# Performance work log

Hardware: AMD Instinct MI355X
Metric: run time of the kernel (lower is better)

## Reference

```python
import jax, jax.numpy as jnp
import numpy as np

N = 50_000
HS = 256
H = 256  # GAT heads (hard-coded in module)
E12 = 250_000
E3 = 500_000


def _gat(x, edge, W, a_src, a_dst, b):
    # PyG GATConv(1, 1, heads=256, concat=False, add_self_loops=False)
    n = x.shape[0]
    xl = x @ W                                   # [N,1]@[1,H] -> [N,H] (out_channels=1 per head)
    src, dst = edge[0], edge[1]
    alpha = jax.nn.leaky_relu((xl * a_src)[src] + (xl * a_dst)[dst], 0.2)  # [E,H]
    amax = jax.ops.segment_max(alpha, dst, num_segments=n)
    ex = jnp.exp(alpha - amax[dst])
    den = jax.ops.segment_sum(ex, dst, num_segments=n)
    w = ex / (den[dst] + 1e-16)                  # per-dst softmax (PyG softmax eps)
    out = jax.ops.segment_sum(xl[src] * w, dst, num_segments=n)            # [N,H]
    return jnp.mean(out, axis=1, keepdims=True) + b                        # concat=False -> head mean


def _sage(x, edge, Wl, Wr):
    # PyG SAGEConv, mean aggregation, root_weight=True, bias=False
    n = x.shape[0]
    src, dst = edge[0], edge[1]
    agg = jax.ops.segment_sum(x[src], dst, num_segments=n)
    cnt = jax.ops.segment_sum(jnp.ones((src.shape[0], 1), x.dtype), dst, num_segments=n)
    return (agg / jnp.maximum(cnt, 1.0)) @ Wl + x @ Wr


def _forward(floats, r1, r2, r3, neg):
    (x, fc1_w, fc1_b, fc2_w, fc2_b, fc3_w, fc3_b,
     g1_w, g1_as, g1_ad, g1_b, g2_w, g2_as, g2_ad, g2_b, g3_w, g3_as, g3_ad, g3_b,
     sg1_wl, sg1_wr, sg2_wl, sg2_wr, sg3_wl, sg3_wr, c21_wl, c21_wr,
     fc4_w, fc4_b, fc4n_w, fc4n_b, fc5_w, fc5_b, fc6_w, fc6_b, fc7_w, fc7_b) = floats
    relu = jax.nn.relu
    x_price = x[:, :1]
    h = relu(x[:, 1:] @ fc1_w + fc1_b)
    h = relu(h @ fc2_w + fc2_b)
    x3 = relu(h @ fc3_w + fc3_b)
    p1 = relu(_gat(x_price, r1, g1_w, g1_as, g1_ad, g1_b))
    p2 = relu(_gat(x_price, r2, g2_w, g2_as, g2_ad, g2_b))
    p3 = relu(_gat(x_price, r3, g3_w, g3_as, g3_ad, g3_b))
    x1 = jnp.concatenate([x3, p1, p2, p3], axis=1)           # [N, hs+3]
    s = jnp.concatenate([
        relu(_sage(x1, r3, sg1_wl, sg1_wr)),
        relu(_sage(x1, r3, sg2_wl, sg2_wr)),
        relu(_sage(x1, r3, sg3_wl, sg3_wr)),
    ], axis=1)                                               # [N, 3*(hs>>1)]
    y = relu(s @ fc4_w + fc4_b)
    y = relu(y @ fc5_w + fc5_b)
    y = y @ fc6_w + fc6_b
    xn = relu(_sage(x1, neg, c21_wl, c21_wr))
    xn = relu(xn @ fc4n_w + fc4n_b)
    xn = xn @ fc7_w + fc7_b
    return (y, xn)


def setup_inputs() -> dict:
    key = jax.random.key(0)
    ks = iter(jax.random.split(key, 64))
    def nrm(shape, s=0.05):
        return jax.random.normal(next(ks), shape, jnp.float32) * s
    def rint(shape, hi):
        return jax.random.randint(next(ks), shape, 0, hi, jnp.int32)
    inp = {
        'x': jax.random.normal(next(ks), (N, 19), jnp.float32),
        'fc1_w': nrm((18, HS)), 'fc1_b': nrm((HS,)),
        'fc2_w': nrm((HS, HS)), 'fc2_b': nrm((HS,)),
        'fc3_w': nrm((HS, HS)), 'fc3_b': nrm((HS,)),
        'g1_w': nrm((1, H)), 'g1_as': nrm((H,)), 'g1_ad': nrm((H,)), 'g1_b': nrm((1,)),
        'g2_w': nrm((1, H)), 'g2_as': nrm((H,)), 'g2_ad': nrm((H,)), 'g2_b': nrm((1,)),
        'g3_w': nrm((1, H)), 'g3_as': nrm((H,)), 'g3_ad': nrm((H,)), 'g3_b': nrm((1,)),
        'sg1_wl': nrm((HS + 3, HS // 2)), 'sg1_wr': nrm((HS + 3, HS // 2)),
        'sg2_wl': nrm((HS + 3, HS // 2)), 'sg2_wr': nrm((HS + 3, HS // 2)),
        'sg3_wl': nrm((HS + 3, HS // 2)), 'sg3_wr': nrm((HS + 3, HS // 2)),
        'c21_wl': nrm((HS + 3, HS)), 'c21_wr': nrm((HS + 3, HS)),
        'fc4_w': nrm((3 * (HS // 2), HS)), 'fc4_b': nrm((HS,)),
        'fc4n_w': nrm((HS, HS)), 'fc4n_b': nrm((HS,)),
        'fc5_w': nrm((HS, HS)), 'fc5_b': nrm((HS,)),
        'fc6_w': nrm((HS, 1)), 'fc6_b': nrm((1,)),
        'fc7_w': nrm((HS, 1)), 'fc7_b': nrm((1,)),
        'r1_edge_index': rint((2, E12), N),
        'r2_edge_index': rint((2, E12), N),
        'r3_edge_index': rint((2, E3), N),
        'neg_edge_index': rint((2, E3), N),
    }
    return inp


def reference(x, fc1_w, fc1_b, fc2_w, fc2_b, fc3_w, fc3_b,
              g1_w, g1_as, g1_ad, g1_b, g2_w, g2_as, g2_ad, g2_b,
              g3_w, g3_as, g3_ad, g3_b,
              sg1_wl, sg1_wr, sg2_wl, sg2_wr, sg3_wl, sg3_wr, c21_wl, c21_wr,
              fc4_w, fc4_b, fc4n_w, fc4n_b, fc5_w, fc5_b, fc6_w, fc6_b, fc7_w, fc7_b,
              r1_edge_index, r2_edge_index, r3_edge_index, neg_edge_index):
    floats = (x, fc1_w, fc1_b, fc2_w, fc2_b, fc3_w, fc3_b,
              g1_w, g1_as, g1_ad, g1_b, g2_w, g2_as, g2_ad, g2_b, g3_w, g3_as, g3_ad, g3_b,
              sg1_wl, sg1_wr, sg2_wl, sg2_wr, sg3_wl, sg3_wr, c21_wl, c21_wr,
              fc4_w, fc4_b, fc4n_w, fc4n_b, fc5_w, fc5_b, fc6_w, fc6_b, fc7_w, fc7_b)
    return _forward(floats, r1_edge_index, r2_edge_index, r3_edge_index, neg_edge_index)
```

## Files before the change

kernel.cpp:

```cpp
#include <hip/hip_runtime.h>
#include <hip/hip_bf16.h>

typedef __hip_bfloat16 bf16;
typedef __attribute__((ext_vector_type(8))) short bfrag;
typedef __attribute__((ext_vector_type(4))) float f32x4;

static constexpr int NN  = 50000;
static constexpr int EA  = 250000;
static constexpr int EB  = 500000;
static constexpr int LDX = 288;

__device__ __forceinline__ float b2f(unsigned int u) { return __uint_as_float((u & 0xffffu) << 16); }
__device__ __forceinline__ unsigned short f2b(float f) {
    bf16 h = __float2bfloat16(f);
    return *reinterpret_cast<unsigned short*>(&h);
}
__device__ __forceinline__ void gload16(const void* g, void* l) {
    __builtin_amdgcn_global_load_lds((const __attribute__((address_space(1))) void*)g,
                                     (__attribute__((address_space(3))) void*)l, 16, 0, 0);
}

__global__ void k_zero(unsigned int* __restrict__ p, int n) {
    int i = blockIdx.x * 256 + threadIdx.x;
    if (i < n) p[i] = 0u;
}

__global__ void k_count(const int* __restrict__ dst, int E, int* __restrict__ deg) {
    int e = blockIdx.x * blockDim.x + threadIdx.x;
    if (e < E) atomicAdd(&deg[dst[e]], 1);
}

__global__ __launch_bounds__(1024) void k_scan4(const int* __restrict__ deg4,
                                                int* __restrict__ rp4,
                                                int* __restrict__ cur4, int n) {
    const int* deg = deg4 + (size_t)blockIdx.x * n;
    int* rp  = rp4  + (size_t)blockIdx.x * (n + 1);
    int* cur = cur4 + (size_t)blockIdx.x * n;
    __shared__ int wsum[16];
    __shared__ int srun;
    int tid = threadIdx.x;
    int lane = tid & 63, wid = tid >> 6;
    if (tid == 0) srun = 0;
    __syncthreads();
    for (int base = 0; base < n; base += 1024) {
        int i = base + tid;
        int v = (i < n) ? deg[i] : 0;
        int incl = v;
        #pragma unroll
        for (int d = 1; d < 64; d <<= 1) {
            int y = __shfl_up(incl, d, 64);
            if (lane >= d) incl += y;
        }
        if (lane == 63) wsum[wid] = incl;
        __syncthreads();
        if (wid == 0 && lane < 16) {
            int w = wsum[lane];
            #pragma unroll
            for (int d = 1; d < 16; d <<= 1) {
                int y = __shfl_up(w, d, 64);
                if (lane >= d) w += y;
            }
            wsum[lane] = w;
        }
        __syncthreads();
        int run  = srun;
        int woff = (wid > 0) ? wsum[wid - 1] : 0;
        int ex   = run + woff + incl - v;
        if (i < n) { rp[i] = ex; cur[i] = ex; }
        int total = wsum[15];
        __syncthreads();
        if (tid == 0) srun = run + total;
        __syncthreads();
    }
    if (tid == 0) rp[n] = srun;
}

__global__ void k_scatter(const int* __restrict__ src, const int* __restrict__ dst, int E,
                          int* __restrict__ cur, int* __restrict__ col) {
    int e = blockIdx.x * blockDim.x + threadIdx.x;
    if (e < E) {
        int p = atomicAdd(&cur[dst[e]], 1);
        col[p] = src[e];
    }
}

__global__ __launch_bounds__(256) void k_fc1(const float* __restrict__ x,
                                             const float* __restrict__ W,
                                             const float* __restrict__ bias,
                                             bf16* __restrict__ out) {
    __shared__ float sx[8][20];
    int tid = threadIdx.x;
    int n0 = blockIdx.x * 8;
    for (int i = tid; i < 8 * 19; i += 256) {
        int m = i / 19, k = i % 19;
        sx[m][k] = x[(size_t)(n0 + m) * 19 + k];
    }
    __syncthreads();
    float wr[18];
    #pragma unroll
    for (int k = 0; k < 18; ++k) wr[k] = W[k * 256 + tid];
    float bv = bias[tid];
    #pragma unroll
    for (int m = 0; m < 8; ++m) {
        float acc = bv;
        #pragma unroll
        for (int k = 0; k < 18; ++k) acc = fmaf(sx[m][k + 1], wr[k], acc);
        out[(size_t)(n0 + m) * 256 + tid] = __float2bfloat16(fmaxf(acc, 0.f));
    }
}

__global__ __launch_bounds__(256) void k_mgemm(
    const bf16* __restrict__ A1, int lda1, int K1,
    const bf16* __restrict__ A2, int lda2, int K2,
    const bf16* __restrict__ WT,
    const float* __restrict__ bias,
    bf16* __restrict__ C, int ldc, int M,
    const float* __restrict__ vdot, float* __restrict__ dotout)
{
    __shared__ char lds[16384] __attribute__((aligned(16)));
    const int tid  = threadIdx.x;
    const int lane = tid & 63;
    const int wid  = tid >> 6;
    const int wm   = wid >> 1, wn = wid & 1;
    const int row0 = blockIdx.y * 128;
    const int col0 = blockIdx.x * 128;
    const int Ktot = K1 + K2;
    const int lmod = lane & 15;
    const int ldiv = lane >> 4;

    f32x4 acc[4][4] = {};

    const bool doA  = (wid < 2);
    const int cbase = (wid & 1) * 4;

    for (int kb = 0; kb < Ktot; kb += 32) {
        __syncthreads();
        if (doA) {
            const bf16* Ap; int lda, kk;
            if (kb < K1) { Ap = A1; lda = lda1; kk = kb; }
            else         { Ap = A2; lda = lda2; kk = kb - K1; }
            int kcol = kk + ldiv * 8;
            #pragma unroll
            for (int c = 0; c < 4; ++c) {
                int chunk = cbase + c;
                int row = row0 + chunk * 16 + lmod;
                row = row < M ? row : M - 1;
                gload16(Ap + (size_t)row * lda + kcol, lds + chunk * 1024);
            }
        } else {
            int kcol = kb + ldiv * 8;
            #pragma unroll
            for (int c = 0; c < 4; ++c) {
                int chunk = cbase + c;
                int col = col0 + chunk * 16 + lmod;
                gload16(WT + (size_t)col * Ktot + kcol, lds + 8192 + chunk * 1024);
            }
        }
        __syncthreads();
        bfrag a[4], b[4];
        #pragma unroll
        for (int i = 0; i < 4; ++i)
            a[i] = *(const bfrag*)(lds + (wm * 4 + i) * 1024 + lane * 16);
        #pragma unroll
        for (int i = 0; i < 4; ++i)
            b[i] = *(const bfrag*)(lds + 8192 + (wn * 4 + i) * 1024 + lane * 16);
        #pragma unroll
        for (int mi = 0; mi < 4; ++mi)
            #pragma unroll
            for (int ni = 0; ni < 4; ++ni)
                acc[mi][ni] = __builtin_amdgcn_mfma_f32_16x16x32_bf16(a[mi], b[ni], acc[mi][ni], 0, 0, 0);
    }

    float bv[4], vv[4];
    #pragma unroll
    for (int ni = 0; ni < 4; ++ni) {
        int colv = col0 + wn * 64 + ni * 16 + lmod;
        bv[ni] = bias ? bias[colv] : 0.f;
        vv[ni] = vdot ? vdot[colv] : 0.f;
    }

    if (vdot) {
        #pragma unroll
        for (int mi = 0; mi < 4; ++mi) {
            #pragma unroll
            for (int r = 0; r < 4; ++r) {
                int row = row0 + wm * 64 + mi * 16 + ldiv * 4 + r;
                float part = 0.f;
                #pragma unroll
                for (int ni = 0; ni < 4; ++ni)
                    part = fmaf(fmaxf(acc[mi][ni][r] + bv[ni], 0.f), vv[ni], part);
                #pragma unroll
                for (int d = 1; d < 16; d <<= 1) part += __shfl_xor(part, d, 64);
                if (lmod == 0 && row < M) atomicAdd(&dotout[row], part);
            }
        }
        return;
    }

    #pragma unroll
    for (int mi = 0; mi < 4; ++mi) {
        int rowb = row0 + wm * 64 + mi * 16 + ldiv * 4;
        #pragma unroll
        for (int ni = 0; ni < 4; ++ni) {
            int col = col0 + wn * 64 + ni * 16 + lmod;
            #pragma unroll
            for (int r = 0; r < 4; ++r) {
                int row = rowb + r;
                if (row < M)
                    C[(size_t)row * ldc + col] = __float2bfloat16(fmaxf(acc[mi][ni][r] + bv[ni], 0.f));
            }
        }
    }
}

__global__ __launch_bounds__(256) void k_gat(
    const float* __restrict__ x,
    const int* __restrict__ rp, const int* __restrict__ col,
    const float* __restrict__ gw, const float* __restrict__ gas,
    const float* __restrict__ gad, const float* __restrict__ gb,
    bf16* __restrict__ x1, int outcol)
{
    int lane = threadIdx.x & 63;
    int node = blockIdx.x * 4 + (threadIdx.x >> 6);
    if (node >= NN) return;
    int beg = rp[node], end = rp[node + 1];
    float bias = gb[0];
    float res;
    if (end == beg) {
        res = fmaxf(bias, 0.f);
    } else {
        float maxa = -3.4e38f, mina = 3.4e38f;
        for (int e = beg + lane; e < end; e += 64) {
            float a = x[(size_t)col[e] * 19];
            maxa = fmaxf(maxa, a);
            mina = fminf(mina, a);
        }
        #pragma unroll
        for (int d = 32; d >= 1; d >>= 1) {
            maxa = fmaxf(maxa, __shfl_xor(maxa, d, 64));
            mina = fminf(mina, __shfl_xor(mina, d, 64));
        }
        float b = x[(size_t)node * 19];
        float w[4], u[4], cc[4];
        #pragma unroll
        for (int j = 0; j < 4; ++j) {
            float wv = gw[lane * 4 + j];
            w[j]  = wv;
            u[j]  = wv * gas[lane * 4 + j];
            cc[j] = b * wv * gad[lane * 4 + j];
        }
        float m[4], s[4], t[4];
        #pragma unroll
        for (int j = 0; j < 4; ++j) {
            float sel = (u[j] >= 0.f) ? maxa : mina;
            float mm = fmaf(sel, u[j], cc[j]);
            m[j] = (mm >= 0.f) ? mm : 0.2f * mm;
            s[j] = 0.f; t[j] = 0.f;
        }
        for (int e = beg; e < end; ++e) {
            float a = x[(size_t)col[e] * 19];
            #pragma unroll
            for (int j = 0; j < 4; ++j) {
                float al = fmaf(a, u[j], cc[j]);
                al = (al >= 0.f) ? al : 0.2f * al;
                float p = __expf(al - m[j]);
                s[j] += p;
                t[j] += p * a;
            }
        }
        float part = 0.f;
        #pragma unroll
        for (int j = 0; j < 4; ++j) part += w[j] * t[j] / (s[j] + 1e-16f);
        #pragma unroll
        for (int d = 32; d >= 1; d >>= 1) part += __shfl_xor(part, d, 64);
        res = fmaxf(part * (1.f / 256.f) + bias, 0.f);
    }
    if (lane == 0) x1[(size_t)node * LDX + outcol] = __float2bfloat16(res);
}

__global__ __launch_bounds__(256) void k_sage_agg(
    const bf16* __restrict__ x1, const int* __restrict__ rp, const int* __restrict__ col,
    bf16* __restrict__ agg)
{
    int lane = threadIdx.x & 63;
    int node = blockIdx.x * 4 + (threadIdx.x >> 6);
    if (node >= NN) return;
    int beg = rp[node], end = rp[node + 1];
    float inv = 1.f / fmaxf((float)(end - beg), 1.f);
    if (lane >= 36) return;
    float s0=0,s1=0,s2=0,s3=0,s4=0,s5=0,s6=0,s7=0;
    for (int e = beg; e < end; ++e) {
        const uint4 v = *(const uint4*)(x1 + (size_t)col[e] * LDX + lane * 8);
        s0 += b2f(v.x); s1 += b2f(v.x >> 16);
        s2 += b2f(v.y); s3 += b2f(v.y >> 16);
        s4 += b2f(v.z); s5 += b2f(v.z >> 16);
        s6 += b2f(v.w); s7 += b2f(v.w >> 16);
    }
    uint4 o;
    o.x = (unsigned)f2b(s0 * inv) | ((unsigned)f2b(s1 * inv) << 16);
    o.y = (unsigned)f2b(s2 * inv) | ((unsigned)f2b(s3 * inv) << 16);
    o.z = (unsigned)f2b(s4 * inv) | ((unsigned)f2b(s5 * inv) << 16);
    o.w = (unsigned)f2b(s6 * inv) | ((unsigned)f2b(s7 * inv) << 16);
    *(uint4*)(agg + (size_t)node * LDX + lane * 8) = o;
}

__global__ void k_final(const float* __restrict__ dots,
                        const float* __restrict__ b6, const float* __restrict__ b7,
                        float* __restrict__ out) {
    int i = blockIdx.x * 256 + threadIdx.x;
    if (i >= 2 * NN) return;
    float b = (i < NN) ? b6[0] : b7[0];
    out[i] = dots[i] + b;
}

__global__ void k_wt(const float* __restrict__ W, bf16* __restrict__ WT, int K, int N) {
    int idx = blockIdx.x * 256 + threadIdx.x;
    if (idx >= K * N) return;
    int n = idx / K, k = idx % K;
    WT[idx] = __float2bfloat16(W[k * N + n]);
}

__global__ void k_wtsage(const float* __restrict__ wl0, const float* __restrict__ wl1,
                         const float* __restrict__ wl2, const float* __restrict__ wr0,
                         const float* __restrict__ wr1, const float* __restrict__ wr2,
                         bf16* __restrict__ WT) {
    int idx = blockIdx.x * 256 + threadIdx.x;
    if (idx >= 384 * 576) return;
    int n = idx / 576, k = idx % 576;
    int half = k / 288, kk = k % 288;
    float v = 0.f;
    if (kk < 259) {
        const float* s = half ? (n < 128 ? wr0 : n < 256 ? wr1 : wr2)
                              : (n < 128 ? wl0 : n < 256 ? wl1 : wl2);
        v = s[kk * 128 + (n & 127)];
    }
    WT[idx] = __float2bfloat16(v);
}

__global__ void k_wtc21(const float* __restrict__ wl, const float* __restrict__ wr,
                        bf16* __restrict__ WT) {
    int idx = blockIdx.x * 256 + threadIdx.x;
    if (idx >= 256 * 576) return;
    int n = idx / 576, k = idx % 576;
    int half = k / 288, kk = k % 288;
    float v = 0.f;
    if (kk < 259) v = (half ? wr : wl)[kk * 256 + n];
    WT[idx] = __float2bfloat16(v);
}

__global__ void k_padx1(bf16* __restrict__ x1) {
    int idx = blockIdx.x * 256 + threadIdx.x;
    if (idx >= NN * 32) return;
    int node = idx >> 5, c = idx & 31;
    x1[(size_t)node * LDX + 256 + c] = __float2bfloat16(0.f);
}

extern "C" void kernel_launch(void* const* d_in, const int* in_sizes, int n_in,
                              void* d_out, int out_size, void* d_ws, size_t ws_size,
                              hipStream_t stream)
{
    (void)in_sizes; (void)n_in; (void)out_size; (void)ws_size;
    const float* x      = (const float*)d_in[0];
    const float* fc1_w  = (const float*)d_in[1];
    const float* fc1_b  = (const float*)d_in[2];
    const float* fc2_w  = (const float*)d_in[3];
    const float* fc2_b  = (const float*)d_in[4];
    const float* fc3_w  = (const float*)d_in[5];
    const float* fc3_b  = (const float*)d_in[6];
    const float* g_w[3]  = {(const float*)d_in[7],  (const float*)d_in[11], (const float*)d_in[15]};
    const float* g_as[3] = {(const float*)d_in[8],  (const float*)d_in[12], (const float*)d_in[16]};
    const float* g_ad[3] = {(const float*)d_in[9],  (const float*)d_in[13], (const float*)d_in[17]};
    const float* g_b[3]  = {(const float*)d_in[10], (const float*)d_in[14], (const float*)d_in[18]};
    const float* sg_wl[3] = {(const float*)d_in[19], (const float*)d_in[21], (const float*)d_in[23]};
    const float* sg_wr[3] = {(const float*)d_in[20], (const float*)d_in[22], (const float*)d_in[24]};
    const float* c21_wl = (const float*)d_in[25];
    const float* c21_wr = (const float*)d_in[26];
    const float* fc4_w  = (const float*)d_in[27];
    const float* fc4_b  = (const float*)d_in[28];
    const float* fc4n_w = (const float*)d_in[29];
    const float* fc4n_b = (const float*)d_in[30];
    const float* fc5_w  = (const float*)d_in[31];
    const float* fc5_b  = (const float*)d_in[32];
    const float* fc6_w  = (const float*)d_in[33];
    const float* fc6_b  = (const float*)d_in[34];
    const float* fc7_w  = (const float*)d_in[35];
    const float* fc7_b  = (const float*)d_in[36];
    const int* eidx[4] = {(const int*)d_in[37], (const int*)d_in[38], (const int*)d_in[39], (const int*)d_in[40]};
    const int  ecnt[4] = {EA, EA, EB, EB};

    bf16* bws = (bf16*)d_ws;
    size_t off = 0;
    bf16* x1    = bws + off; off += (size_t)NN * LDX;
    bf16* bufA  = bws + off; off += (size_t)NN * LDX;
    bf16* bufB  = bws + off; off += (size_t)NN * 384;
    bf16* fc2T  = bws + off; off += 256 * 256;
    bf16* fc3T  = bws + off; off += 256 * 256;
    bf16* fc4T  = bws + off; off += 256 * 384;
    bf16* fc4nT = bws + off; off += 256 * 256;
    bf16* fc5T  = bws + off; off += 256 * 256;
    bf16* sageT = bws + off; off += 384 * 576;
    bf16* c21T  = bws + off; off += 256 * 576;
    float* dots = (float*)(bws + off);
    int* deg4 = (int*)(dots + 2 * NN);
    int* rp4  = deg4 + 4 * NN;
    int* cur4 = rp4 + 4 * (NN + 1);
    int* colx = cur4 + 4 * NN;
    int* colg[4] = {colx, colx + EA, colx + 2 * EA, colx + 2 * EA + EB};

    float* outy = (float*)d_out;

    k_zero<<<(4 * NN + 255) / 256, 256, 0, stream>>>((unsigned int*)deg4, 4 * NN);
    k_zero<<<(2 * NN + 255) / 256, 256, 0, stream>>>((unsigned int*)dots, 2 * NN);

    for (int g = 0; g < 4; ++g)
        k_count<<<(ecnt[g] + 255) / 256, 256, 0, stream>>>(eidx[g] + ecnt[g], ecnt[g], deg4 + g * NN);
    k_scan4<<<4, 1024, 0, stream>>>(deg4, rp4, cur4, NN);
    for (int g = 0; g < 4; ++g)
        k_scatter<<<(ecnt[g] + 255) / 256, 256, 0, stream>>>(eidx[g], eidx[g] + ecnt[g], ecnt[g],
                                                             cur4 + g * NN, colg[g]);

    k_wt<<<(256 * 256 + 255) / 256, 256, 0, stream>>>(fc2_w, fc2T, 256, 256);
    k_wt<<<(256 * 256 + 255) / 256, 256, 0, stream>>>(fc3_w, fc3T, 256, 256);
    k_wt<<<(384 * 256 + 255) / 256, 256, 0, stream>>>(fc4_w, fc4T, 384, 256);
    k_wt<<<(256 * 256 + 255) / 256, 256, 0, stream>>>(fc4n_w, fc4nT, 256, 256);
    k_wt<<<(256 * 256 + 255) / 256, 256, 0, stream>>>(fc5_w, fc5T, 256, 256);
    k_wtsage<<<(384 * 576 + 255) / 256, 256, 0, stream>>>(sg_wl[0], sg_wl[1], sg_wl[2],
                                                          sg_wr[0], sg_wr[1], sg_wr[2], sageT);
    k_wtc21<<<(256 * 576 + 255) / 256, 256, 0, stream>>>(c21_wl, c21_wr, c21T);

    const int gy = (NN + 127) / 128;
    dim3 g2(2, gy), g3(3, gy);

    k_fc1<<<NN / 8, 256, 0, stream>>>(x, fc1_w, fc1_b, bufA);
    k_mgemm<<<g2, 256, 0, stream>>>(bufA, 256, 256, nullptr, 0, 0, fc2T, fc2_b, bufB, 256, NN, nullptr, nullptr);
    k_mgemm<<<g2, 256, 0, stream>>>(bufB, 256, 256, nullptr, 0, 0, fc3T, fc3_b, x1, LDX, NN, nullptr, nullptr);
    k_padx1<<<(NN * 32 + 255) / 256, 256, 0, stream>>>(x1);

    for (int g = 0; g < 3; ++g)
        k_gat<<<NN / 4, 256, 0, stream>>>(x, rp4 + g * (NN + 1), colg[g],
                                          g_w[g], g_as[g], g_ad[g], g_b[g], x1, 256 + g);

    k_sage_agg<<<NN / 4, 256, 0, stream>>>(x1, rp4 + 3 * (NN + 1), colg[3], bufA);
    k_mgemm<<<g2, 256, 0, stream>>>(bufA, LDX, 288, x1, LDX, 288, c21T, nullptr, bufB, 256, NN, nullptr, nullptr);
    k_mgemm<<<g2, 256, 0, stream>>>(bufB, 256, 256, nullptr, 0, 0, fc4nT, fc4n_b, nullptr, 0, NN, fc7_w, dots + NN);

    k_sage_agg<<<NN / 4, 256, 0, stream>>>(x1, rp4 + 2 * (NN + 1), colg[2], bufA);
    k_mgemm<<<g3, 256, 0, stream>>>(bufA, LDX, 288, x1, LDX, 288, sageT, nullptr, bufB, 384, NN, nullptr, nullptr);
    k_mgemm<<<g2, 256, 0, stream>>>(bufB, 384, 384, nullptr, 0, 0, fc4T, fc4_b, bufA, 256, NN, nullptr, nullptr);
    k_mgemm<<<g2, 256, 0, stream>>>(bufA, 256, 256, nullptr, 0, 0, fc5T, fc5_b, nullptr, 0, NN, fc6_w, dots);

    k_final<<<(2 * NN + 255) / 256, 256, 0, stream>>>(dots, fc6_b, fc7_b, outy);
}
```

Measured before the change: 921.5 us.

## Double-buffer GEMM LDS tiles, remap blocks per XCD, stage epilogue via LDS

The GEMM kernel now uses two LDS buffers so the global-to-LDS load for the next K tile is issued while MFMAs run on the current one, with one barrier per iteration instead of two. Workgroup IDs are remapped so consecutive tiles land on the same XCD for better L2 locality. The epilogue writes results to a padded LDS tile and then stores 16-byte vectors per row instead of scattered 2-byte stores. LDS use grows from 16 KB to 36 KB per block, which may reduce occupancy.

```diff
diff --git a/kernel.cpp b/kernel.cpp
--- a/kernel.cpp
+++ b/kernel.cpp
@@ -117,59 +117,76 @@
     bf16* __restrict__ C, int ldc, int M,
     const float* __restrict__ vdot, float* __restrict__ dotout)
 {
-    __shared__ char lds[16384] __attribute__((aligned(16)));
+    __shared__ char lds[36864] __attribute__((aligned(16)));
     const int tid  = threadIdx.x;
     const int lane = tid & 63;
     const int wid  = tid >> 6;
     const int wm   = wid >> 1, wn = wid & 1;
-    const int row0 = blockIdx.y * 128;
-    const int col0 = blockIdx.x * 128;
-    const int Ktot = K1 + K2;
     const int lmod = lane & 15;
     const int ldiv = lane >> 4;
 
-    f32x4 acc[4][4] = {};
-
+    const int gx  = gridDim.x;
+    const int nwg = gx * gridDim.y;
+    const int h   = blockIdx.y * gx + blockIdx.x;
+    const int xcd = h & 7, li = h >> 3;
+    const int q = nwg >> 3, r = nwg & 7;
+    const int t = (xcd < r ? xcd * (q + 1) : r * (q + 1) + (xcd - r) * q) + li;
+    const int row0 = (t / gx) * 128;
+    const int col0 = (t % gx) * 128;
+
+    const int Ktot = K1 + K2;
+    const int nt   = Ktot >> 5;
     const bool doA  = (wid < 2);
     const int cbase = (wid & 1) * 4;
 
-    for (int kb = 0; kb < Ktot; kb += 32) {
-        __syncthreads();
-        if (doA) {
-            const bf16* Ap; int lda, kk;
-            if (kb < K1) { Ap = A1; lda = lda1; kk = kb; }
-            else         { Ap = A2; lda = lda2; kk = kb - K1; }
-            int kcol = kk + ldiv * 8;
-            #pragma unroll
-            for (int c = 0; c < 4; ++c) {
-                int chunk = cbase + c;
-                int row = row0 + chunk * 16 + lmod;
-                row = row < M ? row : M - 1;
-                gload16(Ap + (size_t)row * lda + kcol, lds + chunk * 1024);
-            }
-        } else {
-            int kcol = kb + ldiv * 8;
-            #pragma unroll
-            for (int c = 0; c < 4; ++c) {
-                int chunk = cbase + c;
-                int col = col0 + chunk * 16 + lmod;
-                gload16(WT + (size_t)col * Ktot + kcol, lds + 8192 + chunk * 1024);
-            }
-        }
-        __syncthreads();
+    f32x4 acc[4][4] = {};
+
+    #define STAGE(kb, buf)                                                          \
+    {                                                                               \
+        char* dst = lds + (buf) * 16384;                                            \
+        if (doA) {                                                                  \
+            const bf16* Ap; int lda, kk;                                            \
+            if ((kb) < K1) { Ap = A1; lda = lda1; kk = (kb); }                      \
+            else           { Ap = A2; lda = lda2; kk = (kb) - K1; }                 \
+            int kcol = kk + ldiv * 8;                                               \
+            _Pragma("unroll")                                                       \
+            for (int c = 0; c < 4; ++c) {                                           \
+                int chunk = cbase + c;                                              \
+                int row = row0 + chunk * 16 + lmod;                                 \
+                row = row < M ? row : M - 1;                                        \
+                gload16(Ap + (size_t)row * lda + kcol, dst + chunk * 1024);         \
+            }                                                                       \
+        } else {                                                                    \
+            int kcol = (kb) + ldiv * 8;                                             \
+            _Pragma("unroll")                                                       \
+            for (int c = 0; c < 4; ++c) {                                           \
+                int chunk = cbase + c;                                              \
+                int col = col0 + chunk * 16 + lmod;                                 \
+                gload16(WT + (size_t)col * Ktot + kcol, dst + 8192 + chunk * 1024); \
+            }                                                                       \
+        }                                                                           \
+    }
+
+    STAGE(0, 0);
+    __syncthreads();
+    for (int s = 0; s < nt; ++s) {
+        if (s + 1 < nt) STAGE((s + 1) << 5, (s + 1) & 1);
+        const char* cb = lds + (s & 1) * 16384;
         bfrag a[4], b[4];
         #pragma unroll
         for (int i = 0; i < 4; ++i)
-            a[i] = *(const bfrag*)(lds + (wm * 4 + i) * 1024 + lane * 16);
+            a[i] = *(const bfrag*)(cb + (wm * 4 + i) * 1024 + lane * 16);
         #pragma unroll
         for (int i = 0; i < 4; ++i)
-            b[i] = *(const bfrag*)(lds + 8192 + (wn * 4 + i) * 1024 + lane * 16);
+            b[i] = *(const bfrag*)(cb + 8192 + (wn * 4 + i) * 1024 + lane * 16);
         #pragma unroll
         for (int mi = 0; mi < 4; ++mi)
             #pragma unroll
             for (int ni = 0; ni < 4; ++ni)
                 acc[mi][ni] = __builtin_amdgcn_mfma_f32_16x16x32_bf16(a[mi], b[ni], acc[mi][ni], 0, 0, 0);
-    }
+        __syncthreads();
+    }
+    #undef STAGE
 
     float bv[4], vv[4];
     #pragma unroll
@@ -197,19 +214,25 @@
         return;
     }
 
+    unsigned short* sm = (unsigned short*)lds + (size_t)wid * 4608;
     #pragma unroll
-    for (int mi = 0; mi < 4; ++mi) {
-        int rowb = row0 + wm * 64 + mi * 16 + ldiv * 4;
-        #pragma unroll
-        for (int ni = 0; ni < 4; ++ni) {
-            int col = col0 + wn * 64 + ni * 16 + lmod;
+    for (int mi = 0; mi < 4; ++mi)
+        #pragma unroll
+        for (int ni = 0; ni < 4; ++ni)
             #pragma unroll
             for (int r = 0; r < 4; ++r) {
-                int row = rowb + r;
-                if (row < M)
-                    C[(size_t)row * ldc + col] = __float2bfloat16(fmaxf(acc[mi][ni][r] + bv[ni], 0.f));
+                int rl = mi * 16 + ldiv * 4 + r;
+                int cl = ni * 16 + lmod;
+                sm[rl * 72 + cl] = f2b(fmaxf(acc[mi][ni][r] + bv[ni], 0.f));
             }
-        }
+    #pragma unroll
+    for (int it = 0; it < 8; ++it) {
+        int rl = it * 8 + (lane >> 3);
+        int ck = lane & 7;
+        uint4 v = *(const uint4*)(sm + rl * 72 + ck * 8);
+        int grow = row0 + wm * 64 + rl;
+        if (grow < M)
+            *(uint4*)(C + (size_t)grow * ldc + col0 + wn * 64 + ck * 8) = v;
     }
 }
 
```

Result: faster. 838.6 us (-9.0%).
